# Optimization experiments

Hardware: AMD Instinct MI355X
Metric: run time of the kernel (lower is better)

Reference implementation:

```python
import jax, jax.numpy as jnp
import numpy as np

TEMPERATURE = 0.07
NUM_UNIFY_CLASSES = 256


def setup_inputs() -> dict:
    key = jax.random.key(0)
    k1, k2, k3 = jax.random.split(key, 3)
    b, c, h, w = 16, 256, 128, 128
    # small-magnitude feats so exp(logits) stays finite at temperature 0.07
    feats = jax.random.normal(k1, (b, c, h, w), dtype=jnp.float32) * 0.05
    queue = jax.random.normal(k2, (NUM_UNIFY_CLASSES, c), dtype=jnp.float32)
    queue = queue / jnp.linalg.norm(queue, axis=1, keepdims=True)  # unit rows, as a memory bank would hold
    labels = jax.random.randint(k3, (b * h * w, NUM_UNIFY_CLASSES), 0, 2, dtype=jnp.int32)
    return {"feats": feats, "queue": queue, "labels": labels}


def reference(feats, queue, labels):
    b, c, h, w = feats.shape
    # [b,c,h,w] -> [N, c]
    f = jnp.transpose(feats, (0, 2, 3, 1)).reshape(-1, c)
    # [N, M] logits
    logits = (f @ queue.T) / TEMPERATURE
    pos_mask = labels.reshape(-1, NUM_UNIFY_CLASSES).astype(logits.dtype)
    neg_mask = 1.0 - pos_mask
    sum_neg = jnp.sum(jnp.exp(logits) * neg_mask, axis=1)   # [N]
    sum_pos = jnp.sum(jnp.exp(-logits) * pos_mask, axis=1)  # [N]
    loss = jnp.log(sum_neg * sum_pos + 1.0)                 # [N]
    lb_num = jnp.sum(loss != 0)
    return jnp.where(lb_num == 0, jnp.float32(0.0),
                     jnp.sum(loss) / jnp.maximum(lb_num, 1).astype(loss.dtype))
```

## Files before the change

### kernel.cpp

```cpp
#include <hip/hip_runtime.h>
#include <hip/hip_bf16.h>


typedef __bf16 bf16x8 __attribute__((ext_vector_type(8)));
typedef float floatx4 __attribute__((ext_vector_type(4)));

union BFrag {
  unsigned int u32[4];
  uint4 v;
  bf16x8 bf;
};

__device__ __forceinline__ unsigned int pack_bf2(float a, float b) {
  unsigned int ua = __float_as_uint(a) + 0x8000u;
  unsigned int ub = __float_as_uint(b) + 0x8000u;
  return (ua >> 16) | (ub & 0xffff0000u);
}

__global__ void qprep(const float* __restrict__ queue,
                      unsigned short* __restrict__ qs,
                      float* __restrict__ accum) {
  const int gt = blockIdx.x * 256 + threadIdx.x;
  const int t = gt >> 6;
  const int lane = gt & 63;
  const int m = ((t >> 3) << 4) | (lane & 15);
  const int k0 = ((t & 7) << 5) | ((lane >> 4) << 3);
  const float* qr = queue + m * 256 + k0;
  const float SCALE = 20.6099291556f;
  BFrag u;
#pragma unroll
  for (int j = 0; j < 4; ++j)
    u.u32[j] = pack_bf2(qr[2 * j] * SCALE, qr[2 * j + 1] * SCALE);
  *(uint4*)(qs + (size_t)gt * 8) = u.v;
  if (gt < 128) accum[gt] = 0.0f;
}

__global__ __launch_bounds__(64, 3) void pcl_main(
    const float* __restrict__ feats,
    const int* __restrict__ labels,
    const unsigned short* __restrict__ qs,
    float* __restrict__ accum) {
  const int bx = blockIdx.x;
  const int lane = threadIdx.x & 63;
  const int qd = lane >> 4;
  const int s = lane & 15;

  const int px0 = bx << 4;
  const float* fb = feats + ((size_t)(px0 >> 14) << 22) + (px0 & 16383) + s;
  const int* lp = labels + (((size_t)px0 + s) << 8) + (qd << 2);

  float FA[32], FB[32];
#pragma unroll
  for (int i = 0; i < 32; ++i) {
    const int k = ((i >> 3) << 5) + (qd << 3) + (i & 7);
    FA[i] = fb[(size_t)k << 14];
  }
#pragma unroll
  for (int i = 0; i < 32; ++i) {
    const int k = 128 + ((i >> 3) << 5) + (qd << 3) + (i & 7);
    FB[i] = fb[(size_t)k << 14];
  }
  int4 labP[4], lab1[4], lab2[4], lab3[4];
#pragma unroll
  for (int mt = 0; mt < 4; ++mt)
    labP[mt] = *(const int4*)(lp + (mt << 4));

  BFrag bfr[8];
#pragma unroll
  for (int ks = 0; ks < 4; ++ks)
#pragma unroll
    for (int jj = 0; jj < 4; ++jj)
      bfr[ks].u32[jj] = pack_bf2(FA[ks * 8 + 2 * jj], FA[ks * 8 + 2 * jj + 1]);
#pragma unroll
  for (int ks = 0; ks < 4; ++ks)
#pragma unroll
    for (int jj = 0; jj < 4; ++jj)
      bfr[4 + ks].u32[jj] = pack_bf2(FB[ks * 8 + 2 * jj], FB[ks * 8 + 2 * jj + 1]);

  const uint4* qsv = (const uint4*)qs;
  float nn = 0.0f, pp = 0.0f;

#define DO_CHUNK(C, LB)                                                       \
  do {                                                                        \
    floatx4 acc0 = floatx4{0.f, 0.f, 0.f, 0.f};                               \
    floatx4 acc1 = acc0, acc2 = acc0, acc3 = acc0;                            \
    _Pragma("unroll")                                                         \
    for (int ks = 0; ks < 8; ++ks) {                                          \
      BFrag a0, a1, a2, a3;                                                   \
      a0.v = qsv[((((C) * 4 + 0) * 8 + ks) << 6) + lane];                     \
      a1.v = qsv[((((C) * 4 + 1) * 8 + ks) << 6) + lane];                     \
      a2.v = qsv[((((C) * 4 + 2) * 8 + ks) << 6) + lane];                     \
      a3.v = qsv[((((C) * 4 + 3) * 8 + ks) << 6) + lane];                     \
      acc0 = __builtin_amdgcn_mfma_f32_16x16x32_bf16(a0.bf, bfr[ks].bf, acc0, 0, 0, 0); \
      acc1 = __builtin_amdgcn_mfma_f32_16x16x32_bf16(a1.bf, bfr[ks].bf, acc1, 0, 0, 0); \
      acc2 = __builtin_amdgcn_mfma_f32_16x16x32_bf16(a2.bf, bfr[ks].bf, acc2, 0, 0, 0); \
      acc3 = __builtin_amdgcn_mfma_f32_16x16x32_bf16(a3.bf, bfr[ks].bf, acc3, 0, 0, 0); \
    }                                                                         \
    _Pragma("unroll")                                                         \
    for (int mt = 0; mt < 4; ++mt) {                                          \
      const int4 lb = (LB)[mt];                                               \
      const floatx4 a = (mt == 0) ? acc0 : (mt == 1) ? acc1 : (mt == 2) ? acc2 : acc3; \
      _Pragma("unroll")                                                       \
      for (int r = 0; r < 4; ++r) {                                           \
        const unsigned int y = (unsigned int)((r == 0) ? lb.x : (r == 1) ? lb.y : (r == 2) ? lb.z : lb.w); \
        const float x = __uint_as_float(__float_as_uint(a[r]) ^ (y << 31));   \
        const float e = exp2f(x);                                             \
        nn += y ? 0.0f : e;                                                   \
        pp += y ? e : 0.0f;                                                   \
      }                                                                       \
    }                                                                         \
  } while (0)

#pragma unroll
  for (int mt = 0; mt < 4; ++mt)
    lab1[mt] = *(const int4*)(lp + 64 + (mt << 4));
  DO_CHUNK(0, labP);

#pragma unroll
  for (int mt = 0; mt < 4; ++mt)
    lab2[mt] = *(const int4*)(lp + 128 + (mt << 4));
  DO_CHUNK(1, lab1);

#pragma unroll
  for (int mt = 0; mt < 4; ++mt)
    lab3[mt] = *(const int4*)(lp + 192 + (mt << 4));
  DO_CHUNK(2, lab2);

  DO_CHUNK(3, lab3);
#undef DO_CHUNK

  float sn = nn;
  sn += __shfl_xor(sn, 16);
  sn += __shfl_xor(sn, 32);
  float sp = pp;
  sp += __shfl_xor(sp, 16);
  sp += __shfl_xor(sp, 32);

  float loss_acc = 0.0f, cnt_acc = 0.0f;
  if (lane < 16) {
    const float lg = logf(sn * sp + 1.0f);
    loss_acc = lg;
    cnt_acc = (lg != 0.0f) ? 1.0f : 0.0f;
  }
#pragma unroll
  for (int off = 1; off < 64; off <<= 1) {
    loss_acc += __shfl_xor(loss_acc, off);
    cnt_acc += __shfl_xor(cnt_acc, off);
  }
  if (lane == 0) {
    const int bin = bx & 63;
    atomicAdd(&accum[2 * bin], loss_acc);
    atomicAdd(&accum[2 * bin + 1], cnt_acc);
  }
}

__global__ __launch_bounds__(64) void pcl_finalize(const float* __restrict__ accum,
                                                   float* __restrict__ out) {
  const int lane = threadIdx.x & 63;
  float ssum = accum[2 * lane];
  float c = accum[2 * lane + 1];
#pragma unroll
  for (int off = 1; off < 64; off <<= 1) {
    ssum += __shfl_xor(ssum, off);
    c += __shfl_xor(c, off);
  }
  if (lane == 0) out[0] = (c != 0.0f) ? (ssum / c) : 0.0f;
}

extern "C" void kernel_launch(void* const* d_in, const int* in_sizes, int n_in,
                              void* d_out, int out_size, void* d_ws, size_t ws_size,
                              hipStream_t stream) {
  (void)in_sizes; (void)n_in; (void)out_size; (void)ws_size;
  const float* feats = (const float*)d_in[0];
  const float* queue = (const float*)d_in[1];
  const int* labels = (const int*)d_in[2];

  unsigned short* qs = (unsigned short*)d_ws;
  float* accum = (float*)((char*)d_ws + 256 * 256 * sizeof(unsigned short));

  qprep<<<32, 256, 0, stream>>>(queue, qs, accum);
  pcl_main<<<16384, 64, 0, stream>>>(feats, labels, qs, accum);
  pcl_finalize<<<1, 64, 0, stream>>>(accum, (float*)d_out);
}
```

Measured before the change: 586.6 us.

## Pack four waves per block and prefetch labels two chunks ahead

Each block now holds four independent 64-lane waves, so the grid uses a quarter as many blocks. Label loads are issued two chunks at a time, giving deeper prefetch. Empty asm barriers force the feature loads to complete before the bf16 packing. Launch bounds change from (64,3) to (256,1), which loosens the register limit and may lower occupancy while adding register pressure from the larger label buffers.

```diff
diff --git a/kernel.cpp b/kernel.cpp
--- a/kernel.cpp
+++ b/kernel.cpp
@@ -35,17 +35,19 @@
   if (gt < 128) accum[gt] = 0.0f;
 }
 
-__global__ __launch_bounds__(64, 3) void pcl_main(
+__global__ __launch_bounds__(256, 1) void pcl_main(
     const float* __restrict__ feats,
     const int* __restrict__ labels,
     const unsigned short* __restrict__ qs,
     float* __restrict__ accum) {
-  const int bx = blockIdx.x;
-  const int lane = threadIdx.x & 63;
+  const int tid = threadIdx.x;
+  const int w = tid >> 6;
+  const int lane = tid & 63;
   const int qd = lane >> 4;
   const int s = lane & 15;
 
-  const int px0 = bx << 4;
+  const int wid = (blockIdx.x << 2) | w;
+  const int px0 = wid << 4;
   const float* fb = feats + ((size_t)(px0 >> 14) << 22) + (px0 & 16383) + s;
   const int* lp = labels + (((size_t)px0 + s) << 8) + (qd << 2);
 
@@ -60,10 +62,15 @@
     const int k = 128 + ((i >> 3) << 5) + (qd << 3) + (i & 7);
     FB[i] = fb[(size_t)k << 14];
   }
-  int4 labP[4], lab1[4], lab2[4], lab3[4];
+  int4 LAB01[8];
 #pragma unroll
-  for (int mt = 0; mt < 4; ++mt)
-    labP[mt] = *(const int4*)(lp + (mt << 4));
+  for (int mt = 0; mt < 8; ++mt)
+    LAB01[mt] = *(const int4*)(lp + (mt << 4));
+
+#pragma unroll
+  for (int i = 0; i < 32; ++i) asm volatile("" : "+v"(FA[i]));
+#pragma unroll
+  for (int i = 0; i < 32; ++i) asm volatile("" : "+v"(FB[i]));
 
   BFrag bfr[8];
 #pragma unroll
@@ -80,7 +87,7 @@
   const uint4* qsv = (const uint4*)qs;
   float nn = 0.0f, pp = 0.0f;
 
-#define DO_CHUNK(C, LB)                                                       \
+#define DO_CHUNK(C, ARR, B)                                                   \
   do {                                                                        \
     floatx4 acc0 = floatx4{0.f, 0.f, 0.f, 0.f};                               \
     floatx4 acc1 = acc0, acc2 = acc0, acc3 = acc0;                            \
@@ -98,7 +105,7 @@
     }                                                                         \
     _Pragma("unroll")                                                         \
     for (int mt = 0; mt < 4; ++mt) {                                          \
-      const int4 lb = (LB)[mt];                                               \
+      const int4 lb = (ARR)[(B) + mt];                                        \
       const floatx4 a = (mt == 0) ? acc0 : (mt == 1) ? acc1 : (mt == 2) ? acc2 : acc3; \
       _Pragma("unroll")                                                       \
       for (int r = 0; r < 4; ++r) {                                           \
@@ -111,22 +118,16 @@
     }                                                                         \
   } while (0)
 
+  DO_CHUNK(0, LAB01, 0);
+
+  int4 LAB23[8];
 #pragma unroll
-  for (int mt = 0; mt < 4; ++mt)
-    lab1[mt] = *(const int4*)(lp + 64 + (mt << 4));
-  DO_CHUNK(0, labP);
+  for (int mt = 0; mt < 8; ++mt)
+    LAB23[mt] = *(const int4*)(lp + 128 + (mt << 4));
 
-#pragma unroll
-  for (int mt = 0; mt < 4; ++mt)
-    lab2[mt] = *(const int4*)(lp + 128 + (mt << 4));
-  DO_CHUNK(1, lab1);
-
-#pragma unroll
-  for (int mt = 0; mt < 4; ++mt)
-    lab3[mt] = *(const int4*)(lp + 192 + (mt << 4));
-  DO_CHUNK(2, lab2);
-
-  DO_CHUNK(3, lab3);
+  DO_CHUNK(1, LAB01, 4);
+  DO_CHUNK(2, LAB23, 0);
+  DO_CHUNK(3, LAB23, 4);
 #undef DO_CHUNK
 
   float sn = nn;
@@ -148,7 +149,7 @@
     cnt_acc += __shfl_xor(cnt_acc, off);
   }
   if (lane == 0) {
-    const int bin = bx & 63;
+    const int bin = wid & 63;
     atomicAdd(&accum[2 * bin], loss_acc);
     atomicAdd(&accum[2 * bin + 1], cnt_acc);
   }
@@ -179,6 +180,6 @@
   float* accum = (float*)((char*)d_ws + 256 * 256 * sizeof(unsigned short));
 
   qprep<<<32, 256, 0, stream>>>(queue, qs, accum);
-  pcl_main<<<16384, 64, 0, stream>>>(feats, labels, qs, accum);
+  pcl_main<<<4096, 256, 0, stream>>>(feats, labels, qs, accum);
   pcl_finalize<<<1, 64, 0, stream>>>(accum, (float*)d_out);
 }
```

Result: faster. 568.6 us (-3.1%).
